# Kernel optimization log

Measured on AMD Instinct MI355X. Metric: run time of the kernel, lower is better.

Reference implementation:

```python
import jax, jax.numpy as jnp
import numpy as np

TEMPERATURE = 8.0  # sqrt(head_dim=64)
NEG = -1e30


def setup_inputs() -> dict:
    key = jax.random.key(0)
    kq, kk, kv, kf, km = jax.random.split(key, 5)
    B, H, S, D = 4, 16, 1024, 64
    q = jax.random.normal(kq, (B, H, S, D), dtype=jnp.float32)
    k = jax.random.normal(kk, (B, H, S, D), dtype=jnp.float32)
    v = jax.random.normal(kv, (B, H, S, D), dtype=jnp.float32)
    factor = jax.random.uniform(kf, (B, H, S, 1), dtype=jnp.float32)
    mask = jax.random.randint(km, (B, 1, S, S), 0, 2, dtype=jnp.int32)
    return {"q": q, "k": k, "v": v, "factor": factor, "mask": mask}


def reference(q, k, v, factor, mask):
    # scores = (q * factor / temperature) @ k^T  -> [B, H, S, S]
    scores = jnp.einsum("bhsd,bhtd->bhst", q * (factor / TEMPERATURE), k)
    scores = jnp.where(mask == 0, NEG, scores)
    attn = jax.nn.softmax(scores, axis=-1)  # dropout is identity at eval
    output = jnp.einsum("bhst,bhtd->bhsd", attn, v)
    return (output, attn)
```

## Files before the change

### kernel.cpp

```cpp
#include <hip/hip_runtime.h>
#include <hip/hip_bf16.h>

#define S_ 1024
#define D_ 64
#define QBLK 64
#define THREADS 256
#define LOG2E 1.44269504088896f

typedef __attribute__((ext_vector_type(8)))  short short8;
typedef __attribute__((ext_vector_type(4)))  int   int4v;
typedef __attribute__((ext_vector_type(16))) float f32x16;
typedef __attribute__((ext_vector_type(4)))  float f32x4;

__device__ __forceinline__ unsigned short f2bfu(float x) {
  return __builtin_bit_cast(unsigned short, __float2bfloat16(x));
}

__global__ __launch_bounds__(THREADS) void prep(
    const float* __restrict__ k, const float* __restrict__ v,
    const int* __restrict__ mask, short* __restrict__ kperm,
    short* __restrict__ vperm, unsigned* __restrict__ mw) {
  const int blk = blockIdx.x;
  const int tid = threadIdx.x;
  if (blk < 2048) {
    const int gid = blk * THREADS + tid;
    const int lane = gid & 63;
    const int kc = (gid >> 6) & 3;
    const int t = (gid >> 8) & 31;
    const int bh = gid >> 13;
    const int ln = lane & 31, hi = lane >> 5;
    const float* src = k + ((((size_t)(bh << 10) + (t << 5) + ln)) << 6) + (kc << 4) + (hi << 3);
    f32x4 x0 = *(const f32x4*)src;
    f32x4 x1 = *(const f32x4*)(src + 4);
    short8 o;
#pragma unroll
    for (int i = 0; i < 4; ++i) { o[i] = (short)f2bfu(x0[i]); o[i + 4] = (short)f2bfu(x1[i]); }
    *(short8*)(kperm + ((size_t)gid << 3)) = o;
  } else if (blk < 4096) {
    const int gid = (blk - 2048) * THREADS + tid;
    const int lane = gid & 63;
    const int h = (gid >> 6) & 3;
    const int t = (gid >> 8) & 31;
    const int bh = gid >> 13;
    const int ln = lane & 31, hi = lane >> 5;
    const int dcol = ((h & 2) << 4) + ln;
    const float* vb = v + ((size_t)bh << 16) + dcol;
    short8 o;
#pragma unroll
    for (int i = 0; i < 8; ++i) {
      const int key = (t << 5) + ((h & 1) << 4) + (i & 3) + ((i >> 2) << 3) + (hi << 2);
      o[i] = (short)f2bfu(vb[(size_t)key << 6]);
    }
    *(short8*)(vperm + ((size_t)gid << 3)) = o;
  } else {
    const int g = blk - 4096;
#pragma unroll
    for (int it = 0; it < 8; ++it) {
      const size_t base = ((size_t)g * 8 + it) * THREADS + tid;
      const unsigned long long bal = __ballot(mask[base] != 0);
      if ((tid & 63) == 0) {
        const size_t w2 = base >> 5;
        mw[w2] = (unsigned)bal;
        mw[w2 + 1] = (unsigned)(bal >> 32);
      }
    }
  }
}

__global__ __launch_bounds__(THREADS, 3) void attn_main(
    const float* __restrict__ q, const float* __restrict__ factor,
    const short* __restrict__ kperm, const short* __restrict__ vperm,
    const unsigned* __restrict__ mw, float* __restrict__ out_o,
    float* __restrict__ out_attn) {
  __shared__ float o_red[4][32][D_];
  __shared__ unsigned lds_mw[QBLK * 33];
  __shared__ float rs[4][32];

  const int tid = threadIdx.x;
  const int wave = tid >> 6;
  const int wg = wave >> 1;
  const int wk = wave & 1;
  const int lane = tid & 63;
  const int hi = lane >> 5;
  const int ln = lane & 31;

  const int blk = blockIdx.x;
  const int swz = ((blk & 7) << 7) | (blk >> 3);
  const int qt = swz & 15;
  const int bh = swz >> 4;
  const int b  = bh >> 4;
  const int q0 = qt << 6;

  const short* kpb = kperm + ((size_t)bh << 16);
  const short* vpb = vperm + ((size_t)bh << 16);

  const unsigned* mwb = mw + ((size_t)b << 15) + ((size_t)q0 << 5);
#pragma unroll
  for (int i = tid; i < QBLK * 32; i += THREADS)
    lds_mw[(i >> 5) * 33 + (i & 31)] = mwb[i];

  const size_t qrow = (size_t)bh * S_ + q0 + (wg << 5) + ln;
  const float fs = factor[qrow] * 0.125f * LOG2E;
  const float* qsrc = q + (qrow << 6) + (hi << 3);
  short8 qf[4];
#pragma unroll
  for (int kc = 0; kc < 4; ++kc) {
    f32x4 x0 = *(const f32x4*)(qsrc + (kc << 4));
    f32x4 x1 = *(const f32x4*)(qsrc + (kc << 4) + 4);
    short8 a;
#pragma unroll
    for (int i = 0; i < 4; ++i) { a[i] = (short)f2bfu(x0[i] * fs); a[i + 4] = (short)f2bfu(x1[i] * fs); }
    qf[kc] = a;
  }

  __syncthreads();

  f32x16 oa0, oa1;
#pragma unroll
  for (int i = 0; i < 16; ++i) { oa0[i] = 0.f; oa1[i] = 0.f; }
  float psum = 0.f;

  for (int t = wk; t < 32; t += 2) {
    const short* kt = kpb + ((size_t)t << 11) + (lane << 3);
    const short* vt = vpb + ((size_t)t << 11) + (lane << 3);
    short8 kf[4];
#pragma unroll
    for (int kc = 0; kc < 4; ++kc) kf[kc] = *(const short8*)(kt + (kc << 9));
    const short8 v00 = *(const short8*)(vt);
    const short8 v01 = *(const short8*)(vt + 512);
    const short8 v10 = *(const short8*)(vt + 1024);
    const short8 v11 = *(const short8*)(vt + 1536);
    f32x16 sB;
#pragma unroll
    for (int i = 0; i < 16; ++i) sB[i] = 0.f;
#pragma unroll
    for (int kc = 0; kc < 4; ++kc)
      sB = __builtin_amdgcn_mfma_f32_32x32x16_bf16(kf[kc], qf[kc], sB, 0, 0, 0);
    const unsigned wb = lds_mw[((wg << 5) + ln) * 33 + t];
    int pk[8];
#pragma unroll
    for (int j = 0; j < 8; ++j) {
      const int r0 = 2 * j;
      const int k0 = (r0 & 3) + ((r0 >> 2) << 3) + (hi << 2);
      const float p0 = ((wb >> k0) & 1u) ? __builtin_amdgcn_exp2f(sB[r0]) : 0.f;
      const float p1 = ((wb >> (k0 + 1)) & 1u) ? __builtin_amdgcn_exp2f(sB[r0 + 1]) : 0.f;
      psum += p0 + p1;
      pk[j] = (int)f2bfu(p0) | ((int)f2bfu(p1) << 16);
    }
    int4v lo4 = {pk[0], pk[1], pk[2], pk[3]};
    int4v hi4 = {pk[4], pk[5], pk[6], pk[7]};
    const short8 pa0 = __builtin_bit_cast(short8, lo4);
    const short8 pa1 = __builtin_bit_cast(short8, hi4);
    oa0 = __builtin_amdgcn_mfma_f32_32x32x16_bf16(pa0, v00, oa0, 0, 0, 0);
    oa0 = __builtin_amdgcn_mfma_f32_32x32x16_bf16(pa1, v01, oa0, 0, 0, 0);
    oa1 = __builtin_amdgcn_mfma_f32_32x32x16_bf16(pa0, v10, oa1, 0, 0, 0);
    oa1 = __builtin_amdgcn_mfma_f32_32x32x16_bf16(pa1, v11, oa1, 0, 0, 0);
  }

  psum += __shfl_xor(psum, 32);
  if (lane < 32) rs[wave][ln] = psum;
#pragma unroll
  for (int r = 0; r < 16; ++r) {
    const int row = (r & 3) + ((r >> 2) << 3) + (hi << 2);
    o_red[wave][row][ln] = oa0[r];
    o_red[wave][row][ln + 32] = oa1[r];
  }
  __syncthreads();

  float* op = out_o + (((size_t)bh * S_ + q0) << 6);
#pragma unroll
  for (int it = 0; it < 16; ++it) {
    const int row = (it << 2) + wave;
    const int g2 = (row >> 5) << 1;
    const int rg = row & 31;
    const float il = 1.0f / (rs[g2][rg] + rs[g2 + 1][rg]);
    const float o = o_red[g2][rg][lane] + o_red[g2 + 1][rg][lane];
    __builtin_nontemporal_store(o * il, op + (row << 6) + lane);
  }

  float invr[16];
#pragma unroll
  for (int r = 0; r < 16; ++r) {
    const int row = (r & 3) + ((r >> 2) << 3) + (hi << 2);
    invr[r] = 1.0f / (rs[wg << 1][row] + rs[(wg << 1) + 1][row]);
  }

  float* ap = out_attn + ((size_t)bh << 20) + ((size_t)(q0 + (wg << 5)) << 10);
  for (int t = wk; t < 32; t += 2) {
    const short* kt = kpb + ((size_t)t << 11) + (lane << 3);
    short8 kf[4];
#pragma unroll
    for (int kc = 0; kc < 4; ++kc) kf[kc] = *(const short8*)(kt + (kc << 9));
    f32x16 sA;
#pragma unroll
    for (int i = 0; i < 16; ++i) sA[i] = 0.f;
#pragma unroll
    for (int kc = 0; kc < 4; ++kc)
      sA = __builtin_amdgcn_mfma_f32_32x32x16_bf16(qf[kc], kf[kc], sA, 0, 0, 0);
#pragma unroll
    for (int r = 0; r < 16; ++r) {
      const int row = (r & 3) + ((r >> 2) << 3) + (hi << 2);
      const unsigned w = lds_mw[((wg << 5) + row) * 33 + t];
      const float p = ((w >> ln) & 1u) ? __builtin_amdgcn_exp2f(sA[r]) * invr[r] : 0.f;
      __builtin_nontemporal_store(p, ap + ((size_t)row << 10) + (t << 5) + ln);
    }
  }
}

extern "C" void kernel_launch(void* const* d_in, const int* in_sizes, int n_in,
                              void* d_out, int out_size, void* d_ws, size_t ws_size,
                              hipStream_t stream) {
  (void)in_sizes; (void)n_in; (void)ws_size; (void)out_size;
  const float* q = (const float*)d_in[0];
  const float* k = (const float*)d_in[1];
  const float* v = (const float*)d_in[2];
  const float* f = (const float*)d_in[3];
  const int*   m = (const int*)d_in[4];
  float* out_o    = (float*)d_out;
  float* out_attn = out_o + (size_t)4 * 16 * 1024 * 64;

  short* kpbuf = (short*)d_ws;
  short* vpbuf = kpbuf + 4194304;
  unsigned* mwbuf = (unsigned*)(vpbuf + 4194304);

  prep<<<6144, THREADS, 0, stream>>>(k, v, m, kpbuf, vpbuf, mwbuf);
  attn_main<<<1024, THREADS, 0, stream>>>(q, f, kpbuf, vpbuf, mwbuf, out_o, out_attn);
}
```

Before: 87.29 us.

## Split attention into a row-sum/output kernel and a separate probability-write kernel

The fused kernel is split into two launches. The first computes P·V and the row sums over 32-row query tiles with four waves splitting the key range, and stores the inverse normalizers to workspace. The second recomputes QK^T and writes the normalized attention matrix using those stored normalizers, with a higher occupancy hint. This aims to raise parallelism in the compute phase and isolate the bandwidth-bound attention write, at the cost of an extra launch, recomputing the scores, and reloading Q and the mask.

```diff
diff --git a/kernel.cpp b/kernel.cpp
--- a/kernel.cpp
+++ b/kernel.cpp
@@ -3,7 +3,6 @@
 
 #define S_ 1024
 #define D_ 64
-#define QBLK 64
 #define THREADS 256
 #define LOG2E 1.44269504088896f
 
@@ -67,39 +66,38 @@
   }
 }
 
-__global__ __launch_bounds__(THREADS, 3) void attn_main(
+__global__ __launch_bounds__(THREADS, 3) void attn_sums(
     const float* __restrict__ q, const float* __restrict__ factor,
     const short* __restrict__ kperm, const short* __restrict__ vperm,
     const unsigned* __restrict__ mw, float* __restrict__ out_o,
-    float* __restrict__ out_attn) {
+    float* __restrict__ linv) {
   __shared__ float o_red[4][32][D_];
-  __shared__ unsigned lds_mw[QBLK * 33];
+  __shared__ unsigned lds_mw[32 * 33];
   __shared__ float rs[4][32];
+  __shared__ float inv_l[32];
 
   const int tid = threadIdx.x;
   const int wave = tid >> 6;
-  const int wg = wave >> 1;
-  const int wk = wave & 1;
   const int lane = tid & 63;
   const int hi = lane >> 5;
   const int ln = lane & 31;
 
   const int blk = blockIdx.x;
-  const int swz = ((blk & 7) << 7) | (blk >> 3);
-  const int qt = swz & 15;
-  const int bh = swz >> 4;
+  const int swz = ((blk & 7) << 8) | (blk >> 3);
+  const int qt = swz & 31;
+  const int bh = swz >> 5;
   const int b  = bh >> 4;
-  const int q0 = qt << 6;
+  const int q0 = qt << 5;
 
   const short* kpb = kperm + ((size_t)bh << 16);
   const short* vpb = vperm + ((size_t)bh << 16);
 
   const unsigned* mwb = mw + ((size_t)b << 15) + ((size_t)q0 << 5);
 #pragma unroll
-  for (int i = tid; i < QBLK * 32; i += THREADS)
+  for (int i = tid; i < 32 * 32; i += THREADS)
     lds_mw[(i >> 5) * 33 + (i & 31)] = mwb[i];
 
-  const size_t qrow = (size_t)bh * S_ + q0 + (wg << 5) + ln;
+  const size_t qrow = (size_t)bh * S_ + q0 + ln;
   const float fs = factor[qrow] * 0.125f * LOG2E;
   const float* qsrc = q + (qrow << 6) + (hi << 3);
   short8 qf[4];
@@ -120,7 +118,7 @@
   for (int i = 0; i < 16; ++i) { oa0[i] = 0.f; oa1[i] = 0.f; }
   float psum = 0.f;
 
-  for (int t = wk; t < 32; t += 2) {
+  for (int t = wave; t < 32; t += 4) {
     const short* kt = kpb + ((size_t)t << 11) + (lane << 3);
     const short* vt = vpb + ((size_t)t << 11) + (lane << 3);
     short8 kf[4];
@@ -136,7 +134,7 @@
 #pragma unroll
     for (int kc = 0; kc < 4; ++kc)
       sB = __builtin_amdgcn_mfma_f32_32x32x16_bf16(kf[kc], qf[kc], sB, 0, 0, 0);
-    const unsigned wb = lds_mw[((wg << 5) + ln) * 33 + t];
+    const unsigned wb = lds_mw[ln * 33 + t];
     int pk[8];
 #pragma unroll
     for (int j = 0; j < 8; ++j) {
@@ -167,23 +165,74 @@
   }
   __syncthreads();
 
+  if (tid < 32) {
+    const float il = 1.0f / (rs[0][tid] + rs[1][tid] + rs[2][tid] + rs[3][tid]);
+    inv_l[tid] = il;
+    linv[(size_t)bh * S_ + q0 + tid] = il;
+  }
+  __syncthreads();
+
   float* op = out_o + (((size_t)bh * S_ + q0) << 6);
 #pragma unroll
-  for (int it = 0; it < 16; ++it) {
+  for (int it = 0; it < 8; ++it) {
     const int row = (it << 2) + wave;
-    const int g2 = (row >> 5) << 1;
-    const int rg = row & 31;
-    const float il = 1.0f / (rs[g2][rg] + rs[g2 + 1][rg]);
-    const float o = o_red[g2][rg][lane] + o_red[g2 + 1][rg][lane];
-    __builtin_nontemporal_store(o * il, op + (row << 6) + lane);
-  }
-
+    const float o = o_red[0][row][lane] + o_red[1][row][lane] +
+                    o_red[2][row][lane] + o_red[3][row][lane];
+    __builtin_nontemporal_store(o * inv_l[row], op + (row << 6) + lane);
+  }
+}
+
+__global__ __launch_bounds__(THREADS, 4) void attn_write(
+    const float* __restrict__ q, const float* __restrict__ factor,
+    const short* __restrict__ kperm, const unsigned* __restrict__ mw,
+    const float* __restrict__ linv, float* __restrict__ out_attn) {
+  __shared__ unsigned lds_mw[64 * 33];
+
+  const int tid = threadIdx.x;
+  const int wave = tid >> 6;
+  const int wg = wave >> 1;
+  const int wk = wave & 1;
+  const int lane = tid & 63;
+  const int hi = lane >> 5;
+  const int ln = lane & 31;
+
+  const int blk = blockIdx.x;
+  const int swz = ((blk & 7) << 7) | (blk >> 3);
+  const int qt = swz & 15;
+  const int bh = swz >> 4;
+  const int b  = bh >> 4;
+  const int q0 = qt << 6;
+
+  const short* kpb = kperm + ((size_t)bh << 16);
+
+  const unsigned* mwb = mw + ((size_t)b << 15) + ((size_t)q0 << 5);
+#pragma unroll
+  for (int i = tid; i < 64 * 32; i += THREADS)
+    lds_mw[(i >> 5) * 33 + (i & 31)] = mwb[i];
+
+  const size_t qrow = (size_t)bh * S_ + q0 + (wg << 5) + ln;
+  const float fs = factor[qrow] * 0.125f * LOG2E;
+  const float* qsrc = q + (qrow << 6) + (hi << 3);
+  short8 qf[4];
+#pragma unroll
+  for (int kc = 0; kc < 4; ++kc) {
+    f32x4 x0 = *(const f32x4*)(qsrc + (kc << 4));
+    f32x4 x1 = *(const f32x4*)(qsrc + (kc << 4) + 4);
+    short8 a;
+#pragma unroll
+    for (int i = 0; i < 4; ++i) { a[i] = (short)f2bfu(x0[i] * fs); a[i + 4] = (short)f2bfu(x1[i] * fs); }
+    qf[kc] = a;
+  }
+
+  const float* lp = linv + (size_t)bh * S_ + q0 + (wg << 5);
   float invr[16];
 #pragma unroll
   for (int r = 0; r < 16; ++r) {
     const int row = (r & 3) + ((r >> 2) << 3) + (hi << 2);
-    invr[r] = 1.0f / (rs[wg << 1][row] + rs[(wg << 1) + 1][row]);
-  }
+    invr[r] = lp[row];
+  }
+
+  __syncthreads();
 
   float* ap = out_attn + ((size_t)bh << 20) + ((size_t)(q0 + (wg << 5)) << 10);
   for (int t = wk; t < 32; t += 2) {
@@ -222,7 +271,9 @@
   short* kpbuf = (short*)d_ws;
   short* vpbuf = kpbuf + 4194304;
   unsigned* mwbuf = (unsigned*)(vpbuf + 4194304);
+  float* linv = (float*)(mwbuf + 131072);
 
   prep<<<6144, THREADS, 0, stream>>>(k, v, m, kpbuf, vpbuf, mwbuf);
-  attn_main<<<1024, THREADS, 0, stream>>>(q, f, kpbuf, vpbuf, mwbuf, out_o, out_attn);
-}
+  attn_sums<<<2048, THREADS, 0, stream>>>(q, f, kpbuf, vpbuf, mwbuf, out_o, linv);
+  attn_write<<<1024, THREADS, 0, stream>>>(q, f, kpbuf, mwbuf, linv, out_attn);
+}
```

New measurement: 126.9 us. +45.3%, slower.
